# Kernel optimization log

Hardware: AMD Instinct MI355X
Metric: run time of the kernel (lower is better)

The kernel has to match this reference:

```python
import jax, jax.numpy as jnp
import numpy as np

B, L, D, DFF = 4, 4096, 1024, 4096
EPS = 1e-6

def _rmsnorm(x, w):
    return x * jax.lax.rsqrt(jnp.mean(x * x, axis=-1, keepdims=True) + EPS) * w

def setup_inputs() -> dict:
    key = jax.random.key(0)
    ks = jax.random.split(key, 16)
    s = 1.0 / np.sqrt(D)
    sf = 1.0 / np.sqrt(DFF)
    return {
        "x": jax.random.normal(ks[0], (B, L, D), jnp.float32),
        # QuasiLSTM gate linears, stored [in, out]; y = x @ W + b
        "w_forget": jax.random.normal(ks[1], (D, D), jnp.float32) * s,
        "b_forget": jnp.zeros((D,), jnp.float32),
        "w_input": jax.random.normal(ks[2], (D, D), jnp.float32) * s,
        "b_input": jnp.zeros((D,), jnp.float32),
        "w_igate": jax.random.normal(ks[3], (D, D), jnp.float32) * s,
        "b_igate": jnp.zeros((D,), jnp.float32),
        "w_ogate": jax.random.normal(ks[4], (D, D), jnp.float32) * s,
        "b_ogate": jnp.zeros((D,), jnp.float32),
        "h0": jax.random.normal(ks[5], (D,), jnp.float32),  # last_hidden_init
        "norm1_w": jnp.ones((D,), jnp.float32),
        "norm2_w": jnp.ones((D,), jnp.float32),
        # FFN SwiGLU
        "w_fc": jax.random.normal(ks[6], (D, DFF), jnp.float32) * s,
        "b_fc": jnp.zeros((DFF,), jnp.float32),
        "w_fc_act": jax.random.normal(ks[7], (D, DFF), jnp.float32) * s,
        "b_fc_act": jnp.zeros((DFF,), jnp.float32),
        "w_out": jax.random.normal(ks[8], (DFF, D), jnp.float32) * sf,
        "b_out": jnp.zeros((D,), jnp.float32),
    }

def reference(x, w_forget, b_forget, w_input, b_input, w_igate, b_igate,
              w_ogate, b_ogate, h0, norm1_w, norm2_w,
              w_fc, b_fc, w_fc_act, b_fc_act, w_out, b_out):
    # --- QuasiLSTM branch (pre-norm residual) ---
    x_res = x
    xn = _rmsnorm(x, norm1_w)                                   # [B,L,D]
    forget = jax.nn.sigmoid(xn @ w_forget + b_forget)           # a_t
    inp = jnp.tanh(xn @ w_input + b_input) * jax.nn.sigmoid(xn @ w_igate + b_igate)  # b_t
    # Linear recurrence h_t = a_t * h_{t-1} + b_t, h_0 = 0 (inner chunk),
    # computed as an associative scan over the length axis.
    def comb(left, right):
        a_l, b_l = left
        a_r, b_r = right
        return (a_l * a_r, b_l * a_r + b_r)
    _, h_inner = jax.lax.associative_scan(comb, (forget, inp), axis=1)
    # cross-chunk contribution from last_hidden_init
    h = h_inner + h0[None, None, :] * jnp.cumprod(forget, axis=1)
    y = jnp.tanh(h) * jax.nn.sigmoid(xn @ w_ogate + b_ogate)
    x1 = y + x_res  # dropout p=0 -> identity
    # --- FFN SwiGLU branch ---
    xn2 = _rmsnorm(x1, norm2_w)
    hff = (xn2 @ w_fc + b_fc) * jax.nn.silu(xn2 @ w_fc_act + b_fc_act)
    out = hff @ w_out + b_out
    return out + x1
```

## Files before the change

### kernel.cpp

```cpp
#include <hip/hip_runtime.h>
#include <math.h>
#include <stdint.h>

static constexpr int Bb  = 4;
static constexpr int Ll  = 4096;
static constexpr int Dd  = 1024;
static constexpr int DFF = 4096;
static constexpr int Mm  = Bb * Ll;
static constexpr int CH  = 64;
static constexpr int CS  = Ll / CH;
static constexpr float EPS = 1e-6f;

typedef __attribute__((ext_vector_type(8))) short short8;
typedef __attribute__((ext_vector_type(4))) float floatx4;
typedef __attribute__((ext_vector_type(4))) unsigned short us4;

__device__ __forceinline__ float sigmoidf_(float v) { return 1.0f / (1.0f + __expf(-v)); }
__device__ __forceinline__ float fast_tanh(float x) {
    return 2.0f / (1.0f + __expf(-2.0f * x)) - 1.0f;
}
__device__ __forceinline__ ushort f2bf(float f) {
    union { float f; uint32_t u; } v; v.f = f;
    return (ushort)((v.u + 0x7FFFu + ((v.u >> 16) & 1u)) >> 16);
}
__device__ __forceinline__ float bf2f(ushort h) {
    union { uint32_t u; float f; } v; v.u = (uint32_t)h << 16; return v.f;
}

__device__ __forceinline__ void gload16(const ushort* g, ushort* l) {
    __builtin_amdgcn_global_load_lds(
        (const __attribute__((address_space(1))) uint32_t*)g,
        (__attribute__((address_space(3))) uint32_t*)l, 16, 0, 0);
}

static constexpr int HT_US  = 256 * 32;
static constexpr int BUF_US = 4 * HT_US;

__device__ __forceinline__ void gemm_core_2ph(
    const ushort* __restrict__ A, const ushort* __restrict__ B1,
    const ushort* __restrict__ B2, int m0, int n0b1, int n0b2, int K,
    ushort* lds, floatx4 (&acc1)[8][2], floatx4 (&acc2)[8][2])
{
    const int tid = threadIdx.x;
    const int mm = tid >> 2, ss = tid & 3;
    const int kb = ss ^ ((mm >> 1) & 3);
    const ushort* pA0 = A  + (size_t)(m0 + mm) * K + kb * 8;
    const ushort* pA1 = pA0 + (size_t)128 * K;
    const ushort* pB0 = B1 + (size_t)(n0b1 + mm) * K + kb * 8;
    const ushort* pB1 = B2 + (size_t)(n0b2 + mm) * K + kb * 8;

    const int wave = tid >> 6, lane = tid & 63;
    const int wr = wave >> 2, wc = wave & 3;
    const int fr = lane & 15, q = lane >> 4;
    const int slot8 = (q ^ ((fr >> 1) & 3)) << 3;
    const int aoff  = (wr * 128 + fr) * 32 + slot8;
    const int boff  = 2 * HT_US + (wc * 32 + fr) * 32 + slot8;

    const int NT = K >> 6;

#define STG_TILE(bsel, tt) do { \
        ushort* dA0 = lds + (bsel) * BUF_US; \
        ushort* dA1 = dA0 + HT_US; \
        ushort* dB0 = dA0 + 2 * HT_US; \
        ushort* dB1 = dA0 + 3 * HT_US; \
        int o0 = (tt) * 64, o1 = o0 + 32; \
        gload16(pA0 + o0, dA0 + tid * 8); gload16(pA1 + o0, dA0 + (tid + 512) * 8); \
        gload16(pB0 + o0, dB0 + tid * 8); gload16(pB1 + o0, dB0 + (tid + 512) * 8); \
        gload16(pA0 + o1, dA1 + tid * 8); gload16(pA1 + o1, dA1 + (tid + 512) * 8); \
        gload16(pB0 + o1, dB1 + tid * 8); gload16(pB1 + o1, dB1 + (tid + 512) * 8); } while (0)

#define READ_FRAGS(base) do { \
        _Pragma("unroll") \
        for (int i_ = 0; i_ < 8; ++i_) a[i_] = *(const short8*)&(base)[aoff + i_ * 512]; \
        _Pragma("unroll") \
        for (int n_ = 0; n_ < 2; ++n_) { \
            b[n_] = *(const short8*)&(base)[boff + n_ * 512]; \
            c[n_] = *(const short8*)&(base)[boff + 4096 + n_ * 512]; \
        } } while (0)

#define MFMA_FULL() do { \
        __builtin_amdgcn_s_setprio(1); \
        _Pragma("unroll") \
        for (int mi_ = 0; mi_ < 8; ++mi_) { \
            acc1[mi_][0] = __builtin_amdgcn_mfma_f32_16x16x32_bf16(a[mi_], b[0], acc1[mi_][0], 0, 0, 0); \
            acc2[mi_][0] = __builtin_amdgcn_mfma_f32_16x16x32_bf16(a[mi_], c[0], acc2[mi_][0], 0, 0, 0); \
            acc1[mi_][1] = __builtin_amdgcn_mfma_f32_16x16x32_bf16(a[mi_], b[1], acc1[mi_][1], 0, 0, 0); \
            acc2[mi_][1] = __builtin_amdgcn_mfma_f32_16x16x32_bf16(a[mi_], c[1], acc2[mi_][1], 0, 0, 0); \
        } \
        __builtin_amdgcn_s_setprio(0); } while (0)

    STG_TILE(0, 0);
    asm volatile("s_waitcnt vmcnt(4)" ::: "memory");
    __builtin_amdgcn_s_barrier();

    int t = 0;
    for (; t < NT - 1; ++t) {
        const int buf = t & 1, nbuf = buf ^ 1;
        const ushort* Ab = lds + buf * BUF_US;
        short8 a[8], b[2], c[2];

        READ_FRAGS(Ab);
        STG_TILE(nbuf, t + 1);
        MFMA_FULL();
        asm volatile("s_waitcnt vmcnt(8)" ::: "memory");
        __builtin_amdgcn_s_barrier();

        const ushort* Ab1 = Ab + HT_US;
        READ_FRAGS(Ab1);
        MFMA_FULL();
        asm volatile("s_waitcnt vmcnt(4)" ::: "memory");
        __builtin_amdgcn_s_barrier();
    }
    {
        const int buf = t & 1;
        const ushort* Ab = lds + buf * BUF_US;
        short8 a[8], b[2], c[2];
        READ_FRAGS(Ab);
        MFMA_FULL();
        asm volatile("s_waitcnt vmcnt(0)" ::: "memory");
        __builtin_amdgcn_s_barrier();
        const ushort* Ab1 = Ab + HT_US;
        READ_FRAGS(Ab1);
        MFMA_FULL();
    }
#undef STG_TILE
#undef READ_FRAGS
#undef MFMA_FULL
}

__global__ __launch_bounds__(512) void mfma_gemm_gates(
    const ushort* __restrict__ A, const ushort* __restrict__ W1t,
    const ushort* __restrict__ W2t,
    const float* __restrict__ b_input, const float* __restrict__ b_forget,
    const float* __restrict__ b_igate, const float* __restrict__ b_ogate,
    ushort* __restrict__ Ga, ushort* __restrict__ Gb, ushort* __restrict__ Gog)
{
    __shared__ __align__(16) ushort lds[2 * BUF_US];
    int xcd = blockIdx.x & 7, i = blockIdx.x >> 3;
    int bx = xcd * 2 + (i & 1), by = i >> 1;
    int m0 = by * 256, n0 = bx * 128;

    floatx4 acc1[8][2] = {};
    floatx4 acc2[8][2] = {};
    gemm_core_2ph(A, W1t, W2t, m0, n0, n0, Dd, lds, acc1, acc2);

    int tid = threadIdx.x, wave = tid >> 6, lane = tid & 63;
    int wr = wave >> 2, wc = wave & 3, fr = lane & 15, q = lane >> 4;
    #pragma unroll
    for (int ni = 0; ni < 2; ++ni) {
        int col = n0 + wc * 32 + ni * 16 + fr;
        if (col < 1024) {
            float b1v = b_input[col], b2v = b_igate[col];
            #pragma unroll
            for (int mi = 0; mi < 8; ++mi)
                #pragma unroll
                for (int r = 0; r < 4; ++r) {
                    int row = m0 + wr * 128 + mi * 16 + q * 4 + r;
                    float z1 = acc1[mi][ni][r] + b1v;
                    float z2 = acc2[mi][ni][r] + b2v;
                    Gb[(size_t)row * Dd + col] = f2bf(fast_tanh(z1) * sigmoidf_(z2));
                }
        } else {
            int c2 = col - 1024;
            float b1v = b_forget[c2], b2v = b_ogate[c2];
            #pragma unroll
            for (int mi = 0; mi < 8; ++mi)
                #pragma unroll
                for (int r = 0; r < 4; ++r) {
                    int row = m0 + wr * 128 + mi * 16 + q * 4 + r;
                    float z1 = acc1[mi][ni][r] + b1v;
                    float z2 = acc2[mi][ni][r] + b2v;
                    Ga[(size_t)row * Dd + c2]  = f2bf(sigmoidf_(z1));
                    Gog[(size_t)row * Dd + c2] = f2bf(sigmoidf_(z2));
                }
        }
    }
}

__global__ __launch_bounds__(512) void mfma_gemm_swiglu(
    const ushort* __restrict__ A, const ushort* __restrict__ W1t,
    const float* __restrict__ b1, const ushort* __restrict__ W2t,
    const float* __restrict__ b2, ushort* __restrict__ C)
{
    __shared__ __align__(16) ushort lds[2 * BUF_US];
    int xcd = blockIdx.x & 7, i = blockIdx.x >> 3;
    int bx = xcd * 4 + (i & 3), by = i >> 2;
    int m0 = by * 256, n0 = bx * 128;

    floatx4 acc1[8][2] = {};
    floatx4 acc2[8][2] = {};
    gemm_core_2ph(A, W1t, W2t, m0, n0, n0, Dd, lds, acc1, acc2);

    int tid = threadIdx.x, wave = tid >> 6, lane = tid & 63;
    int wr = wave >> 2, wc = wave & 3, fr = lane & 15, q = lane >> 4;
    #pragma unroll
    for (int ni = 0; ni < 2; ++ni) {
        int col = n0 + wc * 32 + ni * 16 + fr;
        float b1v = b1[col], b2v = b2[col];
        #pragma unroll
        for (int mi = 0; mi < 8; ++mi)
            #pragma unroll
            for (int r = 0; r < 4; ++r) {
                int row = m0 + wr * 128 + mi * 16 + q * 4 + r;
                float z1 = acc1[mi][ni][r] + b1v;
                float z2 = acc2[mi][ni][r] + b2v;
                C[(size_t)row * DFF + col] = f2bf(z1 * z2 * sigmoidf_(z2));
            }
    }
}

__global__ __launch_bounds__(512) void mfma_gemm_residual(
    const ushort* __restrict__ A, const ushort* __restrict__ Wt,
    const float* __restrict__ bias, float* __restrict__ C)
{
    __shared__ __align__(16) ushort lds[2 * BUF_US];
    int xcd = blockIdx.x & 7, i = blockIdx.x >> 3;
    int s = xcd * 32 + i;
    int bx = s & 3, by = s >> 2;
    int m0 = by * 256, n0 = bx * 256;

    floatx4 acc1[8][2] = {};
    floatx4 acc2[8][2] = {};
    gemm_core_2ph(A, Wt, Wt, m0, n0, n0 + 128, DFF, lds, acc1, acc2);

    int tid = threadIdx.x, wave = tid >> 6, lane = tid & 63;
    int wr = wave >> 2, wc = wave & 3, fr = lane & 15, q = lane >> 4;
    #pragma unroll
    for (int ni = 0; ni < 2; ++ni) {
        int col1 = n0 + wc * 32 + ni * 16 + fr;
        int col2 = col1 + 128;
        float bs1 = bias[col1], bs2 = bias[col2];
        #pragma unroll
        for (int mi = 0; mi < 8; ++mi)
            #pragma unroll
            for (int r = 0; r < 4; ++r) {
                int row = m0 + wr * 128 + mi * 16 + q * 4 + r;
                size_t i1 = (size_t)row * Dd + col1;
                size_t i2 = (size_t)row * Dd + col2;
                C[i1] = acc1[mi][ni][r] + bs1 + C[i1];
                C[i2] = acc2[mi][ni][r] + bs2 + C[i2];
            }
    }
}

__global__ __launch_bounds__(256) void transpose_cast_kernel(
    const float* __restrict__ W, ushort* __restrict__ Wt, int K, int N)
{
    __shared__ float t[32][33];
    int lx = threadIdx.x & 31, ly = threadIdx.x >> 5;
    int n = blockIdx.x * 32 + lx;
    #pragma unroll
    for (int i = 0; i < 4; ++i) {
        int k = blockIdx.y * 32 + ly + i * 8;
        t[ly + i * 8][lx] = W[(size_t)k * N + n];
    }
    __syncthreads();
    int k2 = blockIdx.y * 32 + lx;
    #pragma unroll
    for (int i = 0; i < 4; ++i) {
        int n2 = blockIdx.x * 32 + ly + i * 8;
        Wt[(size_t)n2 * K + k2] = f2bf(t[lx][ly + i * 8]);
    }
}

__global__ __launch_bounds__(256) void transpose_cast_gates(
    const float* __restrict__ w_i, const float* __restrict__ w_f,
    const float* __restrict__ w_g, const float* __restrict__ w_o,
    ushort* __restrict__ W1t, ushort* __restrict__ W2t)
{
    int z = blockIdx.z;
    const float* W = (z == 0) ? w_i : (z == 1) ? w_f : (z == 2) ? w_g : w_o;
    ushort* Wt = (z == 0) ? W1t : (z == 1) ? W1t + (size_t)1024 * Dd
               : (z == 2) ? W2t : W2t + (size_t)1024 * Dd;
    __shared__ float t[32][33];
    int lx = threadIdx.x & 31, ly = threadIdx.x >> 5;
    int n = blockIdx.x * 32 + lx;
    #pragma unroll
    for (int i = 0; i < 4; ++i) {
        int k = blockIdx.y * 32 + ly + i * 8;
        t[ly + i * 8][lx] = W[(size_t)k * Dd + n];
    }
    __syncthreads();
    int k2 = blockIdx.y * 32 + lx;
    #pragma unroll
    for (int i = 0; i < 4; ++i) {
        int n2 = blockIdx.x * 32 + ly + i * 8;
        Wt[(size_t)n2 * Dd + k2] = f2bf(t[lx][ly + i * 8]);
    }
}

__global__ __launch_bounds__(256) void rmsnorm_bf16_kernel(
    const float* __restrict__ x, const float* __restrict__ w,
    ushort* __restrict__ o)
{
    int row = blockIdx.x;
    int tid = threadIdx.x;
    float4 v = ((const float4*)(x + (size_t)row * Dd))[tid];
    float ss = v.x*v.x + v.y*v.y + v.z*v.z + v.w*v.w;
    #pragma unroll
    for (int off = 32; off > 0; off >>= 1) ss += __shfl_down(ss, off, 64);
    __shared__ float red[4];
    if ((tid & 63) == 0) red[tid >> 6] = ss;
    __syncthreads();
    float scale = rsqrtf((red[0] + red[1] + red[2] + red[3]) * (1.0f / Dd) + EPS);
    float4 wv = ((const float4*)w)[tid];
    us4 ov;
    ov.x = f2bf(v.x * scale * wv.x);
    ov.y = f2bf(v.y * scale * wv.y);
    ov.z = f2bf(v.z * scale * wv.z);
    ov.w = f2bf(v.w * scale * wv.w);
    *(us4*)&o[(size_t)row * Dd + tid * 4] = ov;
}

__global__ __launch_bounds__(256) void scan_pass1(
    const ushort* __restrict__ Ga, const ushort* __restrict__ Gb,
    float* __restrict__ P, float* __restrict__ Hend)
{
    int tid = threadIdx.x;
    int c = blockIdx.x, b = blockIdx.y;
    size_t base = ((size_t)b * Ll + (size_t)c * CS) * Dd + tid * 4;
    float p[4] = {1.f, 1.f, 1.f, 1.f};
    float h[4] = {};
    #pragma unroll 4
    for (int t = 0; t < CS; ++t) {
        us4 av = *(const us4*)&Ga[base + (size_t)t * Dd];
        us4 bv = *(const us4*)&Gb[base + (size_t)t * Dd];
        #pragma unroll
        for (int j = 0; j < 4; ++j) {
            float aa = bf2f(av[j]);
            float bb = bf2f(bv[j]);
            p[j] *= aa;
            h[j] = aa * h[j] + bb;
        }
    }
    size_t o = ((size_t)b * CH + c) * Dd + tid * 4;
    *(float4*)&P[o]    = make_float4(p[0], p[1], p[2], p[3]);
    *(float4*)&Hend[o] = make_float4(h[0], h[1], h[2], h[3]);
}

__global__ __launch_bounds__(256) void scan_pass2(
    const float* __restrict__ P, const float* __restrict__ Hend,
    const float* __restrict__ h0, float* __restrict__ Carry)
{
    int idx = blockIdx.x * 256 + threadIdx.x;
    int b = idx / Dd, d = idx % Dd;
    float carry = h0[d];
    for (int c = 0; c < CH; ++c) {
        size_t o = ((size_t)b * CH + c) * Dd + d;
        Carry[o] = carry;
        carry = P[o] * carry + Hend[o];
    }
}

__global__ __launch_bounds__(256) void scan_pass3_norm(
    const ushort* __restrict__ Ga, const ushort* __restrict__ Gb,
    const ushort* __restrict__ Gog, const float* __restrict__ Carry,
    const float* __restrict__ x, const float* __restrict__ norm2w,
    float* __restrict__ x1, ushort* __restrict__ xnb)
{
    int tid = threadIdx.x;
    int c = blockIdx.x, b = blockIdx.y;
    size_t base = ((size_t)b * Ll + (size_t)c * CS) * Dd + tid * 4;
    float4 h4 = *(const float4*)&Carry[((size_t)b * CH + c) * Dd + tid * 4];
    float h[4] = {h4.x, h4.y, h4.z, h4.w};
    float4 w4 = ((const float4*)norm2w)[tid];
    float wv[4] = {w4.x, w4.y, w4.z, w4.w};
    __shared__ float red[4];

    for (int t = 0; t < CS; ++t) {
        size_t i = base + (size_t)t * Dd;
        us4 av = *(const us4*)&Ga[i];
        us4 bv = *(const us4*)&Gb[i];
        us4 gv = *(const us4*)&Gog[i];
        float4 xv = *(const float4*)&x[i];
        float xs[4] = {xv.x, xv.y, xv.z, xv.w};
        float v[4];
        #pragma unroll
        for (int j = 0; j < 4; ++j) {
            float aa = bf2f(av[j]);
            float bb = bf2f(bv[j]);
            h[j] = aa * h[j] + bb;
            v[j] = fast_tanh(h[j]) * bf2f(gv[j]) + xs[j];
        }
        *(float4*)&x1[i] = make_float4(v[0], v[1], v[2], v[3]);
        float ss = v[0]*v[0] + v[1]*v[1] + v[2]*v[2] + v[3]*v[3];
        #pragma unroll
        for (int off = 32; off > 0; off >>= 1) ss += __shfl_down(ss, off, 64);
        if ((tid & 63) == 0) red[tid >> 6] = ss;
        __syncthreads();
        float scale = rsqrtf((red[0] + red[1] + red[2] + red[3]) * (1.0f / Dd) + EPS);
        us4 ov;
        #pragma unroll
        for (int j = 0; j < 4; ++j) ov[j] = f2bf(v[j] * scale * wv[j]);
        *(us4*)&xnb[i] = ov;
        __syncthreads();
    }
}

extern "C" void kernel_launch(void* const* d_in, const int* in_sizes, int n_in,
                              void* d_out, int out_size, void* d_ws, size_t ws_size,
                              hipStream_t stream)
{
    const float* x        = (const float*)d_in[0];
    const float* w_forget = (const float*)d_in[1];
    const float* b_forget = (const float*)d_in[2];
    const float* w_input  = (const float*)d_in[3];
    const float* b_input  = (const float*)d_in[4];
    const float* w_igate  = (const float*)d_in[5];
    const float* b_igate  = (const float*)d_in[6];
    const float* w_ogate  = (const float*)d_in[7];
    const float* b_ogate  = (const float*)d_in[8];
    const float* h0       = (const float*)d_in[9];
    const float* norm1_w  = (const float*)d_in[10];
    const float* norm2_w  = (const float*)d_in[11];
    const float* w_fc     = (const float*)d_in[12];
    const float* b_fc     = (const float*)d_in[13];
    const float* w_fc_act = (const float*)d_in[14];
    const float* b_fc_act = (const float*)d_in[15];
    const float* w_out    = (const float*)d_in[16];
    const float* b_out    = (const float*)d_in[17];
    float* out = (float*)d_out;

    char* ws = (char*)d_ws;
    const size_t MB = 1ull << 20;
    ushort* wtG1  = (ushort*)(ws + 0 * MB);
    ushort* wtG2  = (ushort*)(ws + 4 * MB);
    ushort* wtFC  = (ushort*)(ws + 8 * MB);
    ushort* wtFCA = (ushort*)(ws + 16 * MB);
    ushort* wtOUT = (ushort*)(ws + 24 * MB);
    ushort* xnb   = (ushort*)(ws + 32 * MB);
    ushort* Ga    = (ushort*)(ws + 64 * MB);
    ushort* Gb    = (ushort*)(ws + 96 * MB);
    ushort* Gog   = (ushort*)(ws + 128 * MB);
    ushort* hff   = (ushort*)(ws + 64 * MB);
    float*  P     = (float*)(ws + 192 * MB);
    float*  Hend  = (float*)(ws + 193 * MB);
    float*  Carry = (float*)(ws + 194 * MB);

    transpose_cast_gates<<<dim3(32, 32, 4), 256, 0, stream>>>(
        w_input, w_forget, w_igate, w_ogate, wtG1, wtG2);
    transpose_cast_kernel<<<dim3(DFF/32, Dd/32), 256, 0, stream>>>(w_fc,     wtFC,  Dd, DFF);
    transpose_cast_kernel<<<dim3(DFF/32, Dd/32), 256, 0, stream>>>(w_fc_act, wtFCA, Dd, DFF);
    transpose_cast_kernel<<<dim3(Dd/32, DFF/32), 256, 0, stream>>>(w_out,    wtOUT, DFF, Dd);

    rmsnorm_bf16_kernel<<<Mm, 256, 0, stream>>>(x, norm1_w, xnb);

    mfma_gemm_gates<<<(2048/128) * (Mm/256), 512, 0, stream>>>(
        xnb, wtG1, wtG2, b_input, b_forget, b_igate, b_ogate, Ga, Gb, Gog);

    dim3 sg(CH, Bb);
    scan_pass1<<<sg, 256, 0, stream>>>(Ga, Gb, P, Hend);
    scan_pass2<<<(Bb * Dd) / 256, 256, 0, stream>>>(P, Hend, h0, Carry);
    scan_pass3_norm<<<sg, 256, 0, stream>>>(Ga, Gb, Gog, Carry, x, norm2_w,
                                            out, xnb);

    mfma_gemm_swiglu<<<(DFF/128) * (Mm/256), 512, 0, stream>>>(
        xnb, wtFC, b_fc, wtFCA, b_fc_act, hff);

    mfma_gemm_residual<<<(Dd/256) * (Mm/256), 512, 0, stream>>>(
        hff, wtOUT, b_out, out);
}
```

Before: 873.5 us.

## Software-pipeline scan norm, wave-per-row rmsnorm, split LDS fragment reads around staging

Several unrelated changes land together. The GEMM core now reads only the first A fragment and the B/C fragments before issuing the next tile's global loads, then reads the remaining A fragments afterward, to overlap LDS reads with load issue. The first rmsnorm assigns one wave per row and reduces with xor shuffles, which removes the shared-memory reduction and the block barrier. scan_pass3_norm packs two chunks per 512-thread block and double-buffers the reduction slots, so each step needs one barrier instead of two. scan_pass2 uses 64-thread blocks to spread its serial work over more CUs.

```diff
diff --git a/kernel.cpp b/kernel.cpp
--- a/kernel.cpp
+++ b/kernel.cpp
@@ -69,14 +69,15 @@
         gload16(pA0 + o1, dA1 + tid * 8); gload16(pA1 + o1, dA1 + (tid + 512) * 8); \
         gload16(pB0 + o1, dB1 + tid * 8); gload16(pB1 + o1, dB1 + (tid + 512) * 8); } while (0)
 
-#define READ_FRAGS(base) do { \
+#define READ_HEAD(base) do { \
+        a[0] = *(const short8*)&(base)[aoff]; \
+        b[0] = *(const short8*)&(base)[boff]; \
+        c[0] = *(const short8*)&(base)[boff + 4096]; \
+        b[1] = *(const short8*)&(base)[boff + 512]; \
+        c[1] = *(const short8*)&(base)[boff + 4096 + 512]; } while (0)
+#define READ_TAIL(base) do { \
         _Pragma("unroll") \
-        for (int i_ = 0; i_ < 8; ++i_) a[i_] = *(const short8*)&(base)[aoff + i_ * 512]; \
-        _Pragma("unroll") \
-        for (int n_ = 0; n_ < 2; ++n_) { \
-            b[n_] = *(const short8*)&(base)[boff + n_ * 512]; \
-            c[n_] = *(const short8*)&(base)[boff + 4096 + n_ * 512]; \
-        } } while (0)
+        for (int i_ = 1; i_ < 8; ++i_) a[i_] = *(const short8*)&(base)[aoff + i_ * 512]; } while (0)
 
 #define MFMA_FULL() do { \
         __builtin_amdgcn_s_setprio(1); \
@@ -99,14 +100,16 @@
         const ushort* Ab = lds + buf * BUF_US;
         short8 a[8], b[2], c[2];
 
-        READ_FRAGS(Ab);
+        READ_HEAD(Ab);
         STG_TILE(nbuf, t + 1);
+        READ_TAIL(Ab);
         MFMA_FULL();
         asm volatile("s_waitcnt vmcnt(8)" ::: "memory");
         __builtin_amdgcn_s_barrier();
 
         const ushort* Ab1 = Ab + HT_US;
-        READ_FRAGS(Ab1);
+        READ_HEAD(Ab1);
+        READ_TAIL(Ab1);
         MFMA_FULL();
         asm volatile("s_waitcnt vmcnt(4)" ::: "memory");
         __builtin_amdgcn_s_barrier();
@@ -115,16 +118,19 @@
         const int buf = t & 1;
         const ushort* Ab = lds + buf * BUF_US;
         short8 a[8], b[2], c[2];
-        READ_FRAGS(Ab);
+        READ_HEAD(Ab);
+        READ_TAIL(Ab);
         MFMA_FULL();
         asm volatile("s_waitcnt vmcnt(0)" ::: "memory");
         __builtin_amdgcn_s_barrier();
         const ushort* Ab1 = Ab + HT_US;
-        READ_FRAGS(Ab1);
+        READ_HEAD(Ab1);
+        READ_TAIL(Ab1);
         MFMA_FULL();
     }
 #undef STG_TILE
-#undef READ_FRAGS
+#undef READ_HEAD
+#undef READ_TAIL
 #undef MFMA_FULL
 }
 
@@ -293,23 +299,29 @@
     const float* __restrict__ x, const float* __restrict__ w,
     ushort* __restrict__ o)
 {
-    int row = blockIdx.x;
-    int tid = threadIdx.x;
-    float4 v = ((const float4*)(x + (size_t)row * Dd))[tid];
-    float ss = v.x*v.x + v.y*v.y + v.z*v.z + v.w*v.w;
-    #pragma unroll
-    for (int off = 32; off > 0; off >>= 1) ss += __shfl_down(ss, off, 64);
-    __shared__ float red[4];
-    if ((tid & 63) == 0) red[tid >> 6] = ss;
-    __syncthreads();
-    float scale = rsqrtf((red[0] + red[1] + red[2] + red[3]) * (1.0f / Dd) + EPS);
-    float4 wv = ((const float4*)w)[tid];
-    us4 ov;
-    ov.x = f2bf(v.x * scale * wv.x);
-    ov.y = f2bf(v.y * scale * wv.y);
-    ov.z = f2bf(v.z * scale * wv.z);
-    ov.w = f2bf(v.w * scale * wv.w);
-    *(us4*)&o[(size_t)row * Dd + tid * 4] = ov;
+    int wave = threadIdx.x >> 6, lane = threadIdx.x & 63;
+    int row = blockIdx.x * 4 + wave;
+    const float4* xr = (const float4*)(x + (size_t)row * Dd);
+    float4 v[4];
+    float ss = 0.f;
+    #pragma unroll
+    for (int j = 0; j < 4; ++j) {
+        v[j] = xr[lane + j * 64];
+        ss += v[j].x * v[j].x + v[j].y * v[j].y + v[j].z * v[j].z + v[j].w * v[j].w;
+    }
+    #pragma unroll
+    for (int off = 1; off < 64; off <<= 1) ss += __shfl_xor(ss, off, 64);
+    float scale = rsqrtf(ss * (1.0f / Dd) + EPS);
+    #pragma unroll
+    for (int j = 0; j < 4; ++j) {
+        float4 wv = ((const float4*)w)[lane + j * 64];
+        us4 ov;
+        ov.x = f2bf(v[j].x * scale * wv.x);
+        ov.y = f2bf(v[j].y * scale * wv.y);
+        ov.z = f2bf(v[j].z * scale * wv.z);
+        ov.w = f2bf(v[j].w * scale * wv.w);
+        *(us4*)&o[(size_t)row * Dd + (lane + j * 64) * 4] = ov;
+    }
 }
 
 __global__ __launch_bounds__(256) void scan_pass1(
@@ -338,11 +350,11 @@
     *(float4*)&Hend[o] = make_float4(h[0], h[1], h[2], h[3]);
 }
 
-__global__ __launch_bounds__(256) void scan_pass2(
+__global__ __launch_bounds__(64) void scan_pass2(
     const float* __restrict__ P, const float* __restrict__ Hend,
     const float* __restrict__ h0, float* __restrict__ Carry)
 {
-    int idx = blockIdx.x * 256 + threadIdx.x;
+    int idx = blockIdx.x * 64 + threadIdx.x;
     int b = idx / Dd, d = idx % Dd;
     float carry = h0[d];
     for (int c = 0; c < CH; ++c) {
@@ -352,29 +364,29 @@
     }
 }
 
-__global__ __launch_bounds__(256) void scan_pass3_norm(
+__global__ __launch_bounds__(512) void scan_pass3_norm(
     const ushort* __restrict__ Ga, const ushort* __restrict__ Gb,
     const ushort* __restrict__ Gog, const float* __restrict__ Carry,
     const float* __restrict__ x, const float* __restrict__ norm2w,
     float* __restrict__ x1, ushort* __restrict__ xnb)
 {
     int tid = threadIdx.x;
-    int c = blockIdx.x, b = blockIdx.y;
-    size_t base = ((size_t)b * Ll + (size_t)c * CS) * Dd + tid * 4;
-    float4 h4 = *(const float4*)&Carry[((size_t)b * CH + c) * Dd + tid * 4];
+    int half = tid >> 8, ltid = tid & 255;
+    int c = blockIdx.x * 2 + half, b = blockIdx.y;
+    size_t base = ((size_t)b * Ll + (size_t)c * CS) * Dd + ltid * 4;
+    float4 h4 = *(const float4*)&Carry[((size_t)b * CH + c) * Dd + ltid * 4];
     float h[4] = {h4.x, h4.y, h4.z, h4.w};
-    float4 w4 = ((const float4*)norm2w)[tid];
+    float4 w4 = ((const float4*)norm2w)[ltid];
     float wv[4] = {w4.x, w4.y, w4.z, w4.w};
-    __shared__ float red[4];
-
-    for (int t = 0; t < CS; ++t) {
-        size_t i = base + (size_t)t * Dd;
-        us4 av = *(const us4*)&Ga[i];
-        us4 bv = *(const us4*)&Gb[i];
-        us4 gv = *(const us4*)&Gog[i];
-        float4 xv = *(const float4*)&x[i];
+    __shared__ float red[2][2][4];
+
+    float v[4];
+    {
+        us4 av = *(const us4*)&Ga[base];
+        us4 bv = *(const us4*)&Gb[base];
+        us4 gv = *(const us4*)&Gog[base];
+        float4 xv = *(const float4*)&x[base];
         float xs[4] = {xv.x, xv.y, xv.z, xv.w};
-        float v[4];
         #pragma unroll
         for (int j = 0; j < 4; ++j) {
             float aa = bf2f(av[j]);
@@ -382,17 +394,43 @@
             h[j] = aa * h[j] + bb;
             v[j] = fast_tanh(h[j]) * bf2f(gv[j]) + xs[j];
         }
-        *(float4*)&x1[i] = make_float4(v[0], v[1], v[2], v[3]);
+        *(float4*)&x1[base] = make_float4(v[0], v[1], v[2], v[3]);
         float ss = v[0]*v[0] + v[1]*v[1] + v[2]*v[2] + v[3]*v[3];
         #pragma unroll
         for (int off = 32; off > 0; off >>= 1) ss += __shfl_down(ss, off, 64);
-        if ((tid & 63) == 0) red[tid >> 6] = ss;
-        __syncthreads();
-        float scale = rsqrtf((red[0] + red[1] + red[2] + red[3]) * (1.0f / Dd) + EPS);
+        if ((ltid & 63) == 0) red[0][half][ltid >> 6] = ss;
+    }
+    __syncthreads();
+
+    for (int t = 0; t < CS; ++t) {
+        int p = t & 1;
+        float scale = rsqrtf((red[p][half][0] + red[p][half][1] +
+                              red[p][half][2] + red[p][half][3]) * (1.0f / Dd) + EPS);
         us4 ov;
         #pragma unroll
         for (int j = 0; j < 4; ++j) ov[j] = f2bf(v[j] * scale * wv[j]);
-        *(us4*)&xnb[i] = ov;
+        *(us4*)&xnb[base + (size_t)t * Dd] = ov;
+
+        if (t + 1 < CS) {
+            size_t i = base + (size_t)(t + 1) * Dd;
+            us4 av = *(const us4*)&Ga[i];
+            us4 bv = *(const us4*)&Gb[i];
+            us4 gv = *(const us4*)&Gog[i];
+            float4 xv = *(const float4*)&x[i];
+            float xs[4] = {xv.x, xv.y, xv.z, xv.w};
+            #pragma unroll
+            for (int j = 0; j < 4; ++j) {
+                float aa = bf2f(av[j]);
+                float bb = bf2f(bv[j]);
+                h[j] = aa * h[j] + bb;
+                v[j] = fast_tanh(h[j]) * bf2f(gv[j]) + xs[j];
+            }
+            *(float4*)&x1[i] = make_float4(v[0], v[1], v[2], v[3]);
+            float ss = v[0]*v[0] + v[1]*v[1] + v[2]*v[2] + v[3]*v[3];
+            #pragma unroll
+            for (int off = 32; off > 0; off >>= 1) ss += __shfl_down(ss, off, 64);
+            if ((ltid & 63) == 0) red[(t + 1) & 1][half][ltid >> 6] = ss;
+        }
         __syncthreads();
     }
 }
@@ -443,16 +481,16 @@
     transpose_cast_kernel<<<dim3(DFF/32, Dd/32), 256, 0, stream>>>(w_fc_act, wtFCA, Dd, DFF);
     transpose_cast_kernel<<<dim3(Dd/32, DFF/32), 256, 0, stream>>>(w_out,    wtOUT, DFF, Dd);
 
-    rmsnorm_bf16_kernel<<<Mm, 256, 0, stream>>>(x, norm1_w, xnb);
+    rmsnorm_bf16_kernel<<<Mm / 4, 256, 0, stream>>>(x, norm1_w, xnb);
 
     mfma_gemm_gates<<<(2048/128) * (Mm/256), 512, 0, stream>>>(
         xnb, wtG1, wtG2, b_input, b_forget, b_igate, b_ogate, Ga, Gb, Gog);
 
     dim3 sg(CH, Bb);
     scan_pass1<<<sg, 256, 0, stream>>>(Ga, Gb, P, Hend);
-    scan_pass2<<<(Bb * Dd) / 256, 256, 0, stream>>>(P, Hend, h0, Carry);
-    scan_pass3_norm<<<sg, 256, 0, stream>>>(Ga, Gb, Gog, Carry, x, norm2_w,
-                                            out, xnb);
+    scan_pass2<<<(Bb * Dd) / 64, 64, 0, stream>>>(P, Hend, h0, Carry);
+    scan_pass3_norm<<<dim3(CH / 2, Bb), 512, 0, stream>>>(
+        Ga, Gb, Gog, Carry, x, norm2_w, out, xnb);
 
     mfma_gemm_swiglu<<<(DFF/128) * (Mm/256), 512, 0, stream>>>(
         xnb, wtFC, b_fc, wtFCA, b_fc_act, hff);
```

Measured after the change: 886.8 us. About the same (+1.5%).
